# Kernel tuning notes

Hardware: AMD Instinct MI355X
Metric: run time of the kernel (lower is better)

Reference implementation:

```python
import jax, jax.numpy as jnp
import numpy as np

LN_EPS = 1e-5

def _layer_norm(x, gamma, beta):
    mu = jnp.mean(x, axis=-1, keepdims=True)
    var = jnp.mean(jnp.square(x - mu), axis=-1, keepdims=True)
    return (x - mu) * jax.lax.rsqrt(var + LN_EPS) * gamma + beta

def setup_inputs() -> dict:
    key = jax.random.key(0)
    ks = jax.random.split(key, 6)
    B, Lc, S, H = 8, 16384, 2048, 256
    char_embeddings = jax.random.normal(ks[0], (B, Lc, H), dtype=jnp.float32)
    # include some negative indices (-1, -2) to exercise the no-token mask path
    token_alignment = jax.random.randint(ks[1], (B, Lc), -2, S, dtype=jnp.int32).astype(jnp.int64)
    decoder_hidden_states = jax.random.normal(ks[2], (B, S, H), dtype=jnp.float32)
    scale1 = 1.0 / np.sqrt(2 * H)
    W1 = jax.random.normal(ks[3], (2 * H, H), dtype=jnp.float32) * scale1
    b1 = jnp.zeros((H,), dtype=jnp.float32)
    W2 = jax.random.normal(ks[4], (2 * H, H), dtype=jnp.float32) * scale1
    b2 = jnp.zeros((H,), dtype=jnp.float32)
    ln_gamma = jnp.ones((H,), dtype=jnp.float32)
    ln_beta = jnp.zeros((H,), dtype=jnp.float32)
    return {
        "char_embeddings": char_embeddings,
        "token_alignment": token_alignment,
        "decoder_hidden_states": decoder_hidden_states,
        "W1": W1, "b1": b1, "W2": W2, "b2": b2,
        "ln_gamma": ln_gamma, "ln_beta": ln_beta,
    }

def reference(char_embeddings, token_alignment, decoder_hidden_states,
              W1, b1, W2, b2, ln_gamma, ln_beta):
    B, Lc, H = char_embeddings.shape
    S = decoder_hidden_states.shape[1]
    # per-character gather of decoder token representations (vectorized over batch)
    valid_idx = jnp.clip(token_alignment, 0, S - 1)                         # [B, Lc]
    tok_reprs = jnp.take_along_axis(decoder_hidden_states,
                                    valid_idx[..., None].astype(jnp.int32),
                                    axis=1)                                  # [B, Lc, H]
    tok_reprs = jnp.where((token_alignment < 0)[..., None], 0.0, tok_reprs)
    # alignment_network: Linear(2H -> H)
    combined = jnp.concatenate([char_embeddings, tok_reprs], axis=-1)        # [B, Lc, 2H]
    aligned = jnp.einsum('blk,kh->blh', combined, W1) + b1                   # [B, Lc, H]
    # syllable_feature_extractor: Linear(2H->H) + LayerNorm + GELU (+ eval-mode Dropout)
    combined2 = jnp.concatenate([char_embeddings, aligned], axis=-1)         # [B, Lc, 2H]
    feats = jnp.einsum('blk,kh->blh', combined2, W2) + b2
    feats = _layer_norm(feats, ln_gamma, ln_beta)
    feats = jax.nn.gelu(feats, approximate=False)                            # torch nn.GELU exact
    return char_embeddings + feats
```

## Files before the change

### kernel.cpp

```cpp
#include <hip/hip_runtime.h>
#include <hip/hip_bf16.h>
#include <math.h>
#include <stdint.h>

#define H     256
#define K2    512
#define SDEC  2048
#define LCSH  14
#define BM    64
#define BK    64
#define NTHR  256

typedef __attribute__((ext_vector_type(8))) short  short8;
typedef __attribute__((ext_vector_type(4))) float  f32x4;

__device__ __forceinline__ unsigned short f2bf(float f) {
  union { float f; unsigned int u; } c; c.f = f;
  unsigned int u = c.u;
  unsigned int r = u + 0x7fffu + ((u >> 16) & 1u);
  return (unsigned short)(r >> 16);
}

__global__ __launch_bounds__(256) void fuse_weights(
    const float* __restrict__ W1, const float* __restrict__ W2,
    unsigned short* __restrict__ wft) {
  __shared__ float As[64][65];
  __shared__ float Bs[64][65];
  const int t  = threadIdx.x;
  const int k0 = (blockIdx.x >> 2) * 64;
  const int n0 = (blockIdx.x & 3) * 64;
  const int lr = t >> 2;
  const int ls = t & 3;
  const int tk = t >> 4;
  const int tn = t & 15;

  float acc[4][4];
#pragma unroll
  for (int i = 0; i < 4; ++i)
#pragma unroll
    for (int c = 0; c < 4; ++c) acc[i][c] = 0.0f;

  for (int jt = 0; jt < 4; ++jt) {
    const int j0 = jt * 64;
    __syncthreads();
    const float* a_src = W1 + (size_t)(k0 + lr) * H + j0 + ls * 16;
    const float* b_src = W2 + (size_t)(H + j0 + lr) * H + n0 + ls * 16;
#pragma unroll
    for (int i = 0; i < 16; ++i) {
      As[lr][ls * 16 + i] = a_src[i];
      Bs[lr][ls * 16 + i] = b_src[i];
    }
    __syncthreads();
#pragma unroll 8
    for (int j = 0; j < 64; ++j) {
      float a[4], b[4];
#pragma unroll
      for (int i = 0; i < 4; ++i) a[i] = As[tk * 4 + i][j];
#pragma unroll
      for (int c = 0; c < 4; ++c) b[c] = Bs[j][tn * 4 + c];
#pragma unroll
      for (int i = 0; i < 4; ++i)
#pragma unroll
        for (int c = 0; c < 4; ++c) acc[i][c] += a[i] * b[c];
    }
  }

#pragma unroll
  for (int i = 0; i < 4; ++i) {
    const int k = k0 + tk * 4 + i;
#pragma unroll
    for (int c = 0; c < 4; ++c) {
      const int n = n0 + tn * 4 + c;
      float v = acc[i][c];
      if (k < H) v += W2[(size_t)k * H + n];
      wft[(size_t)n * K2 + k] = f2bf(v);
    }
  }
}

__global__ __launch_bounds__(256) void fuse_bias(
    const float* __restrict__ W2, const float* __restrict__ b1,
    const float* __restrict__ b2, float* __restrict__ biasf) {
  const int n = threadIdx.x;
  float acc = b2[n];
  for (int j = 0; j < H; ++j) acc += b1[j] * W2[(size_t)(H + j) * H + n];
  biasf[n] = acc;
}

__global__ __launch_bounds__(NTHR, 3) void syl_main(
    const float* __restrict__ cemb, const int* __restrict__ tal,
    const float* __restrict__ dec, const unsigned short* __restrict__ wft,
    const float* __restrict__ biasf, const float* __restrict__ gamma,
    const float* __restrict__ beta, float* __restrict__ out) {

  __shared__ __align__(16) char smem[16640];
  unsigned short* AshC = (unsigned short*)smem;
  float* Ef = (float*)smem;

  __shared__ int   idxs[BM];
  __shared__ float msks[BM];
  __shared__ float stats[4][BM][2];

  const int t    = threadIdx.x;
  const int wave = t >> 6;
  const int lane = t & 63;
  const int quad = lane >> 4;
  const int l15  = lane & 15;
  const int row0 = blockIdx.x * BM;
  const int bidx = row0 >> LCSH;
  const float* decb = dec + (size_t)bidx * SDEC * H;

  if (t < BM) {
    int ix = tal[row0 + t];
    idxs[t] = ix < 0 ? 0 : (ix >= SDEC ? SDEC - 1 : ix);
    msks[t] = ix < 0 ? 0.0f : 1.0f;
  }

  f32x4 acc[4][4];
#pragma unroll
  for (int m = 0; m < 4; ++m)
#pragma unroll
    for (int n = 0; n < 4; ++n) acc[m][n] = (f32x4){0.f, 0.f, 0.f, 0.f};

  const int srow = t >> 2;
  const int sseg = t & 3;
  const int ksS  = sseg >> 1;
  const int qS   = (sseg & 1) * 2;
  const int mS   = srow >> 4;
  const int l15S = srow & 15;
  const int wchunk0 = (ksS * 4 + mS) * 64 + qS * 16 + l15S;

  {
    const float* src = cemb + (size_t)(row0 + srow) * H + sseg * 16;
    float4 f[4];
#pragma unroll
    for (int q = 0; q < 4; ++q) f[q] = *(const float4*)(src + q * 4);
    unsigned short hb[16];
#pragma unroll
    for (int q = 0; q < 4; ++q) {
      hb[q * 4 + 0] = f2bf(f[q].x); hb[q * 4 + 1] = f2bf(f[q].y);
      hb[q * 4 + 2] = f2bf(f[q].z); hb[q * 4 + 3] = f2bf(f[q].w);
    }
    *(short8*)(AshC + (size_t)wchunk0 * 8)        = *(short8*)&hb[0];
    *(short8*)(AshC + (size_t)(wchunk0 + 16) * 8) = *(short8*)&hb[8];
  }
  __syncthreads();

  int buf = 0;
  for (int ki = 0; ki < 8; ++ki) {
    const int k0 = ki * BK;

    short8 bf[2][4];
#pragma unroll
    for (int ks = 0; ks < 2; ++ks)
#pragma unroll
      for (int n = 0; n < 4; ++n) {
        const unsigned short* bp =
            wft + (size_t)(wave * 64 + n * 16 + l15) * K2 + k0 + ks * 32 + quad * 8;
        bf[ks][n] = *(const short8*)bp;
      }

    float4 f[4];
    float scale = 1.0f;
    if (ki < 7) {
      const int k0n = k0 + BK;
      const float* src;
      if (k0n < H) {
        src = cemb + (size_t)(row0 + srow) * H + k0n + sseg * 16;
      } else {
        src = decb + (size_t)idxs[srow] * H + (k0n - H) + sseg * 16;
        scale = msks[srow];
      }
#pragma unroll
      for (int q = 0; q < 4; ++q) f[q] = *(const float4*)(src + q * 4);
    }

#pragma unroll
    for (int ks = 0; ks < 2; ++ks) {
      short8 af[4];
#pragma unroll
      for (int m = 0; m < 4; ++m)
        af[m] = *(const short8*)(AshC +
                 (size_t)(((buf * 2 + ks) * 4 + m) * 64 + lane) * 8);
#pragma unroll
      for (int n = 0; n < 4; ++n)
#pragma unroll
        for (int m = 0; m < 4; ++m)
          acc[m][n] = __builtin_amdgcn_mfma_f32_16x16x32_bf16(
              af[m], bf[ks][n], acc[m][n], 0, 0, 0);
    }

    if (ki < 7) {
      unsigned short hb[16];
#pragma unroll
      for (int q = 0; q < 4; ++q) {
        hb[q * 4 + 0] = f2bf(f[q].x * scale); hb[q * 4 + 1] = f2bf(f[q].y * scale);
        hb[q * 4 + 2] = f2bf(f[q].z * scale); hb[q * 4 + 3] = f2bf(f[q].w * scale);
      }
      const int nb = buf ^ 1;
      *(short8*)(AshC + (size_t)(nb * 512 + wchunk0) * 8)      = *(short8*)&hb[0];
      *(short8*)(AshC + (size_t)(nb * 512 + wchunk0 + 16) * 8) = *(short8*)&hb[8];
      __syncthreads();
      buf = nb;
    }
  }

  float bvals[4], gvals[4], betv[4];
#pragma unroll
  for (int n = 0; n < 4; ++n) {
    const int col = wave * 64 + n * 16 + l15;
    bvals[n] = biasf[col];
    gvals[n] = gamma[col];
    betv[n]  = beta[col];
  }
#pragma unroll
  for (int m = 0; m < 4; ++m)
#pragma unroll
    for (int n = 0; n < 4; ++n)
#pragma unroll
      for (int r = 0; r < 4; ++r) acc[m][n][r] += bvals[n];

#pragma unroll
  for (int m = 0; m < 4; ++m)
#pragma unroll
    for (int r = 0; r < 4; ++r) {
      float a = 0.f, b = 0.f;
#pragma unroll
      for (int n = 0; n < 4; ++n) {
        const float v = acc[m][n][r];
        a += v; b += v * v;
      }
#pragma unroll
      for (int d = 1; d < 16; d <<= 1) {
        a += __shfl_xor(a, d, 64);
        b += __shfl_xor(b, d, 64);
      }
      if (l15 == 0) {
        const int row = m * 16 + quad * 4 + r;
        stats[wave][row][0] = a;
        stats[wave][row][1] = b;
      }
    }
  __syncthreads();

  float mean_[4][4], rstd_[4][4];
#pragma unroll
  for (int m = 0; m < 4; ++m)
#pragma unroll
    for (int r = 0; r < 4; ++r) {
      const int row = m * 16 + quad * 4 + r;
      const float a = stats[0][row][0] + stats[1][row][0] +
                      stats[2][row][0] + stats[3][row][0];
      const float b = stats[0][row][1] + stats[1][row][1] +
                      stats[2][row][1] + stats[3][row][1];
      const float mu  = a * (1.0f / 256.0f);
      const float var = b * (1.0f / 256.0f) - mu * mu;
      mean_[m][r] = mu;
      rstd_[m][r] = rsqrtf(var + 1e-5f);
    }

  const int erow = t >> 4;
  const int eseg = t & 15;
#pragma unroll
  for (int m = 0; m < 4; ++m) {
#pragma unroll
    for (int r = 0; r < 4; ++r) {
#pragma unroll
      for (int n = 0; n < 4; ++n) {
        const float x = (acc[m][n][r] - mean_[m][r]) * rstd_[m][r];
        const float y = x * gvals[n] + betv[n];
        const float g = 0.5f * y * (1.0f + erff(y * 0.70710678118654752f));
        Ef[(quad * 4 + r) * 260 + wave * 64 + n * 16 + l15] = g;
      }
    }
    __syncthreads();
    {
      const size_t grow = (size_t)row0 + m * 16 + erow;
      const float* crow = cemb + grow * H + eseg * 16;
      float* orow = out + grow * H + eseg * 16;
#pragma unroll
      for (int j = 0; j < 4; ++j) {
        float4 v = *(const float4*)&Ef[erow * 260 + eseg * 16 + j * 4];
        float4 c = *(const float4*)(crow + j * 4);
        v.x += c.x; v.y += c.y; v.z += c.z; v.w += c.w;
        *(float4*)(orow + j * 4) = v;
      }
    }
    __syncthreads();
  }
}

extern "C" void kernel_launch(void* const* d_in, const int* in_sizes, int n_in,
                              void* d_out, int out_size, void* d_ws, size_t ws_size,
                              hipStream_t stream) {
  const float* cemb  = (const float*)d_in[0];
  const int*   tal   = (const int*)d_in[1];
  const float* dec   = (const float*)d_in[2];
  const float* W1    = (const float*)d_in[3];
  const float* b1    = (const float*)d_in[4];
  const float* W2    = (const float*)d_in[5];
  const float* b2    = (const float*)d_in[6];
  const float* gamma = (const float*)d_in[7];
  const float* beta  = (const float*)d_in[8];
  float* out = (float*)d_out;

  unsigned short* wft = (unsigned short*)d_ws;
  float* biasf = (float*)((char*)d_ws + (size_t)K2 * H * sizeof(unsigned short));

  const int rows = in_sizes[0] / H;

  hipLaunchKernelGGL(fuse_weights, dim3(32), dim3(256), 0, stream, W1, W2, wft);
  hipLaunchKernelGGL(fuse_bias, dim3(1), dim3(256), 0, stream, W2, b1, b2, biasf);
  hipLaunchKernelGGL(syl_main, dim3(rows / BM), dim3(NTHR), 0, stream,
                     cemb, tal, dec, wft, biasf, gamma, beta, out);
}
```

Baseline: 406.8 us.

## Merge bias prep into weight-fusion kernel, raise occupancy, remap blocks across XCDs

Folds the bias-fusion kernel into an extra block of the weight-fusion kernel, removing one launch, and gives its dot product four independent accumulators. Raises the main kernel's launch-bounds minimum blocks per SM from 3 to 6, which pushes the compiler toward fewer registers and risks spills. Remaps block IDs so consecutive row tiles land on the same XCD, which is meant to improve L2 locality for the decoder-state gathers within a batch.

```diff
diff --git a/kernel.cpp b/kernel.cpp
--- a/kernel.cpp
+++ b/kernel.cpp
@@ -23,7 +23,22 @@
 
 __global__ __launch_bounds__(256) void fuse_weights(
     const float* __restrict__ W1, const float* __restrict__ W2,
-    unsigned short* __restrict__ wft) {
+    const float* __restrict__ b1, const float* __restrict__ b2,
+    unsigned short* __restrict__ wft, float* __restrict__ biasf) {
+  if (blockIdx.x == 32) {
+    const int n = threadIdx.x;
+    float a0 = b2[n], a1 = 0.f, a2 = 0.f, a3 = 0.f;
+#pragma unroll 4
+    for (int j = 0; j < H; j += 4) {
+      a0 += b1[j + 0] * W2[(size_t)(H + j + 0) * H + n];
+      a1 += b1[j + 1] * W2[(size_t)(H + j + 1) * H + n];
+      a2 += b1[j + 2] * W2[(size_t)(H + j + 2) * H + n];
+      a3 += b1[j + 3] * W2[(size_t)(H + j + 3) * H + n];
+    }
+    biasf[n] = (a0 + a1) + (a2 + a3);
+    return;
+  }
+
   __shared__ float As[64][65];
   __shared__ float Bs[64][65];
   const int t  = threadIdx.x;
@@ -78,16 +93,7 @@
   }
 }
 
-__global__ __launch_bounds__(256) void fuse_bias(
-    const float* __restrict__ W2, const float* __restrict__ b1,
-    const float* __restrict__ b2, float* __restrict__ biasf) {
-  const int n = threadIdx.x;
-  float acc = b2[n];
-  for (int j = 0; j < H; ++j) acc += b1[j] * W2[(size_t)(H + j) * H + n];
-  biasf[n] = acc;
-}
-
-__global__ __launch_bounds__(NTHR, 3) void syl_main(
+__global__ __launch_bounds__(NTHR, 6) void syl_main(
     const float* __restrict__ cemb, const int* __restrict__ tal,
     const float* __restrict__ dec, const unsigned short* __restrict__ wft,
     const float* __restrict__ biasf, const float* __restrict__ gamma,
@@ -106,7 +112,12 @@
   const int lane = t & 63;
   const int quad = lane >> 4;
   const int l15  = lane & 15;
-  const int row0 = blockIdx.x * BM;
+
+  const int nwg  = gridDim.x;
+  const int bid  = ((nwg & 7) == 0)
+                     ? (int)((blockIdx.x & 7) * (nwg >> 3) + (blockIdx.x >> 3))
+                     : (int)blockIdx.x;
+  const int row0 = bid * BM;
   const int bidx = row0 >> LCSH;
   const float* decb = dec + (size_t)bidx * SDEC * H;
 
@@ -309,8 +320,8 @@
 
   const int rows = in_sizes[0] / H;
 
-  hipLaunchKernelGGL(fuse_weights, dim3(32), dim3(256), 0, stream, W1, W2, wft);
-  hipLaunchKernelGGL(fuse_bias, dim3(1), dim3(256), 0, stream, W2, b1, b2, biasf);
+  hipLaunchKernelGGL(fuse_weights, dim3(33), dim3(256), 0, stream,
+                     W1, W2, b1, b2, wft, biasf);
   hipLaunchKernelGGL(syl_main, dim3(rows / BM), dim3(NTHR), 0, stream,
                      cemb, tal, dec, wft, biasf, gamma, beta, out);
 }
```

Result: slower. 879.1 us (+116.1%).
